# Kernel tuning notes

Hardware: AMD Instinct MI355X
Metric: run time of the kernel (lower is better)

The kernel has to match this reference:

```python
import jax, jax.numpy as jnp
import numpy as np

H = 128          # hid_feats
IN0, IN1 = 128, 64
OUT = 64         # out_feats
L = 3            # num_layers
N = 50000        # nodes per graph


def _rbf(x, W, b):
    # sklearn RBFSampler: z = sqrt(2/D) * cos(x @ W + b)
    return jnp.sqrt(2.0 / H) * jnp.cos(x @ W + b)


def _sage_branch(feat, src, dst, Wself, Wneigh, bias, n_nodes):
    # deg of each dst node (constant across layers)
    deg = jax.ops.segment_sum(jnp.ones_like(dst, dtype=feat.dtype), dst, n_nodes)
    denom = jnp.maximum(deg, 1.0)[:, None]
    for i in range(Wself.shape[0]):
        s = jax.ops.segment_sum(feat[src], dst, n_nodes)   # gather + scatter-add
        neigh = jnp.where(deg[:, None] > 0, s / denom, 0.0)
        feat = feat @ Wself[i] + neigh @ Wneigh[i] + bias[i]
    return feat


def setup_inputs() -> dict:
    key = jax.random.key(0)
    ks = jax.random.split(key, 20)
    gamma = 0.1
    inp = {}
    inp['feat0'] = jax.random.normal(ks[0], (N, IN0), jnp.float32)
    inp['feat1'] = jax.random.normal(ks[1], (N, IN1), jnp.float32)
    E = 800000
    inp['src0'] = jax.random.randint(ks[2], (E,), 0, N, jnp.int32)
    inp['dst0'] = jax.random.randint(ks[3], (E,), 0, N, jnp.int32)
    inp['src1'] = jax.random.randint(ks[4], (E,), 0, N, jnp.int32)
    inp['dst1'] = jax.random.randint(ks[5], (E,), 0, N, jnp.int32)
    # RBF random Fourier feature params (W ~ sqrt(2*gamma)*N(0,1), b ~ U[0,2pi))
    inp['rbf_W0'] = jnp.sqrt(2 * gamma) * jax.random.normal(ks[6], (IN0, H), jnp.float32)
    inp['rbf_b0'] = jax.random.uniform(ks[7], (H,), jnp.float32, 0.0, 2 * np.pi)
    inp['rbf_W1'] = jnp.sqrt(2 * gamma) * jax.random.normal(ks[8], (IN1, H), jnp.float32)
    inp['rbf_b1'] = jax.random.uniform(ks[9], (H,), jnp.float32, 0.0, 2 * np.pi)
    sc = 1.0 / np.sqrt(H)
    # branch 1 (g1) and branch 2 (g0) SAGEConv params, stacked over layers
    inp['Wself1'] = sc * jax.random.normal(ks[10], (L, H, H), jnp.float32)
    inp['Wneigh1'] = sc * jax.random.normal(ks[11], (L, H, H), jnp.float32)
    inp['b1'] = jnp.zeros((L, H), jnp.float32)
    inp['Wself2'] = sc * jax.random.normal(ks[12], (L, H, H), jnp.float32)
    inp['Wneigh2'] = sc * jax.random.normal(ks[13], (L, H, H), jnp.float32)
    inp['b2'] = jnp.zeros((L, H), jnp.float32)
    inp['fc1_W'] = sc * jax.random.normal(ks[14], (2 * H, H), jnp.float32)
    inp['fc1_b'] = jnp.zeros((H,), jnp.float32)
    inp['out_W'] = sc * jax.random.normal(ks[15], (H, OUT), jnp.float32)
    inp['out_b'] = jnp.zeros((OUT,), jnp.float32)
    inp['ro_W'] = (1.0 / np.sqrt(OUT)) * jax.random.normal(ks[16], (OUT, 1), jnp.float32)
    inp['ro_b'] = jnp.zeros((1,), jnp.float32)
    return inp


def reference(feat0, feat1, src0, dst0, src1, dst1,
              rbf_W0, rbf_b0, rbf_W1, rbf_b1,
              Wself1, Wneigh1, b1, Wself2, Wneigh2, b2,
              fc1_W, fc1_b, out_W, out_b, ro_W, ro_b):
    # branch 1: g1 path-complex features
    h1 = _rbf(feat1, rbf_W1, rbf_b1)
    y1 = _sage_branch(h1, src1, dst1, Wself1, Wneigh1, b1, feat1.shape[0])
    # branch 2: g0 node features
    h0 = _rbf(feat0, rbf_W0, rbf_b0)
    y2 = _sage_branch(h0, src0, dst0, Wself2, Wneigh2, b2, feat0.shape[0])
    # adaptive_avg_pool1d to 1 == mean over nodes
    y = jnp.concatenate([y2.mean(axis=0), y1.mean(axis=0)], axis=0)  # [2H]
    h = jax.nn.relu(y @ fc1_W + fc1_b)          # dropout is identity in eval
    h = jax.nn.leaky_relu(h @ out_W + out_b, negative_slope=0.01)
    return h @ ro_W + ro_b                      # [1]
```

## Files before the change

### kernel.cpp

```cpp
#include <hip/hip_runtime.h>
#include <math.h>

#define HF   128
#define CAPW 64
#define HB   64

__global__ __launch_bounds__(256) void histgemm_kernel(const float* __restrict__ A,
                                                       const float* __restrict__ W,
                                                       const float* __restrict__ bias,
                                                       float* __restrict__ hout,
                                                       float* __restrict__ partial,
                                                       const int* __restrict__ s0, const int* __restrict__ d0,
                                                       const int* __restrict__ s1, const int* __restrict__ d1,
                                                       unsigned int* __restrict__ cntbuf,
                                                       int N, int E, int histBlocks){
  __shared__ __align__(16) unsigned int sm32[12544];

  const int t = threadIdx.x;
  const int HW = (N + 3) >> 2;

  if ((int)blockIdx.x < histBlocks){
    const int bid = blockIdx.x;
    const int b  = bid & 63;
    const int br = (bid >> 6) & 1;
    const int z  = bid >> 7;
    const int* keys = z ? (br ? d1 : d0) : (br ? s1 : s0);
    for (int w = t; w < HW; w += 256) sm32[w] = 0u;
    __syncthreads();
    const int C  = (E + HB - 1) / HB;
    const int lo = b * C;
    int hi = lo + C; if (hi > E) hi = E;
    for (int i = lo + t; i < hi; i += 256){
      int k = keys[i];
      atomicAdd(&sm32[k >> 2], 1u << ((k & 3) << 3));
    }
    __syncthreads();
    unsigned int* out = cntbuf + ((size_t)(z * 2 + br) * HB + b) * HW;
    for (int w = t; w < HW; w += 256) out[w] = sm32[w];
    return;
  }

  float (*As)[68]   = (float(*)[68])sm32;
  float (*Bs)[132]  = (float(*)[132])((float*)sm32 + 1088);
  float (*red)[128] = (float(*)[128])sm32;
  const int tx = t & 15;
  const int ty = t >> 4;
  const int rb = (int)blockIdx.x - histBlocks;
  const int rowbase = rb << 6;

  float acc[4][8];
  #pragma unroll
  for (int i = 0; i < 4; ++i)
    #pragma unroll
    for (int j = 0; j < 8; ++j) acc[i][j] = 0.f;

  const int ar = t >> 2;
  const int ac = (t & 3) << 2;
  const int arow = rowbase + ar;
  const int bk0 = t >> 5;
  const int bc0 = (t & 31) << 2;

  for (int k0 = 0; k0 < 128; k0 += 16){
    __syncthreads();
    float4 av = make_float4(0.f, 0.f, 0.f, 0.f);
    if (arow < N) av = *(const float4*)&A[(size_t)arow * 128 + (k0 + ac)];
    As[ac + 0][ar] = av.x; As[ac + 1][ar] = av.y;
    As[ac + 2][ar] = av.z; As[ac + 3][ar] = av.w;
    float4 b0 = *(const float4*)&W[(size_t)(k0 + bk0) * HF + bc0];
    float4 b1 = *(const float4*)&W[(size_t)(k0 + bk0 + 8) * HF + bc0];
    *(float4*)&Bs[bk0][bc0]     = b0;
    *(float4*)&Bs[bk0 + 8][bc0] = b1;
    __syncthreads();
    #pragma unroll
    for (int kk = 0; kk < 16; ++kk){
      const float4 a  = *(const float4*)&As[kk][ty << 2];
      const float4 p0 = *(const float4*)&Bs[kk][tx << 2];
      const float4 p1 = *(const float4*)&Bs[kk][64 + (tx << 2)];
      const float aa[4] = {a.x, a.y, a.z, a.w};
      const float bb[8] = {p0.x, p0.y, p0.z, p0.w, p1.x, p1.y, p1.z, p1.w};
      #pragma unroll
      for (int i = 0; i < 4; ++i)
        #pragma unroll
        for (int j = 0; j < 8; ++j)
          acc[i][j] = fmaf(aa[i], bb[j], acc[i][j]);
    }
  }

  const float4 bia0 = *(const float4*)&bias[tx << 2];
  const float4 bia1 = *(const float4*)&bias[64 + (tx << 2)];
  const float bb0[8] = {bia0.x, bia0.y, bia0.z, bia0.w, bia1.x, bia1.y, bia1.z, bia1.w};
  float o[4][8];
  float cw[8];
  #pragma unroll
  for (int j = 0; j < 8; ++j) cw[j] = 0.f;
  #pragma unroll
  for (int i = 0; i < 4; ++i){
    int row = rowbase + (ty << 2) + i;
    bool valid = row < N;
    #pragma unroll
    for (int j = 0; j < 8; ++j){
      o[i][j] = 0.125f * cosf(acc[i][j] + bb0[j]);
      if (valid) cw[j] += o[i][j];
    }
    if (valid){
      *(float4*)&hout[(size_t)row * HF + (tx << 2)]      = make_float4(o[i][0], o[i][1], o[i][2], o[i][3]);
      *(float4*)&hout[(size_t)row * HF + 64 + (tx << 2)] = make_float4(o[i][4], o[i][5], o[i][6], o[i][7]);
    }
  }

  __syncthreads();
  #pragma unroll
  for (int j = 0; j < 4; ++j){
    red[ty][(tx << 2) + j]      = cw[j];
    red[ty][64 + (tx << 2) + j] = cw[4 + j];
  }
  __syncthreads();
  for (int off = 8; off; off >>= 1){
    if (ty < off){
      #pragma unroll
      for (int j = 0; j < 4; ++j){
        red[ty][(tx << 2) + j]      += red[ty + off][(tx << 2) + j];
        red[ty][64 + (tx << 2) + j] += red[ty + off][64 + (tx << 2) + j];
      }
    }
    __syncthreads();
  }
  if (ty == 0){
    #pragma unroll
    for (int j = 0; j < 4; ++j){
      partial[(size_t)rb * 512 + (tx << 2) + j]      = red[0][(tx << 2) + j];
      partial[(size_t)rb * 512 + 64 + (tx << 2) + j] = red[0][64 + (tx << 2) + j];
    }
  }
}

__global__ __launch_bounds__(256) void scan_kernel(unsigned int* __restrict__ cntbuf,
                                                   int* __restrict__ deg,
                                                   int* __restrict__ fill, int N){
  int k = blockIdx.x * 256 + threadIdx.x;
  if (k >= 2 * N) return;
  const int br = k >= N;
  const int kk = k - br * N;
  const int HW = (N + 3) >> 2;
  unsigned char* cb = (unsigned char*)cntbuf;
  size_t dbase = ((size_t)(2 + br) * HB) * HW * 4 + kk;
  int ds = 0;
  for (int b = 0; b < HB; ++b) ds += cb[dbase + (size_t)b * HW * 4];
  deg[k] = ds;
  size_t sbase = ((size_t)(0 + br) * HB) * HW * 4 + kk;
  int run = 0;
  for (int b = 0; b < HB; ++b){
    size_t a = sbase + (size_t)b * HW * 4;
    int c = cb[a];
    cb[a] = (unsigned char)run;
    run += c;
  }
  fill[k] = run;
}

__global__ __launch_bounds__(256) void scatter_kernel(const int* __restrict__ s0, const int* __restrict__ d0,
                                                      const int* __restrict__ s1, const int* __restrict__ d1,
                                                      const unsigned int* __restrict__ cntbuf,
                                                      unsigned short* __restrict__ slots,
                                                      int N, int E){
  __shared__ unsigned int sm32[12544];
  const int t  = threadIdx.x;
  const int b  = blockIdx.x & 63;
  const int br = blockIdx.x >> 6;
  const int HW = (N + 3) >> 2;
  const unsigned int* offw = cntbuf + ((size_t)br * HB + b) * HW;
  for (int w = t; w < HW; w += 256) sm32[w] = offw[w];
  __syncthreads();
  const int* srcA = br ? s1 : s0;
  const int* dstA = br ? d1 : d0;
  const int C  = (E + HB - 1) / HB;
  const int lo = b * C;
  int hi = lo + C; if (hi > E) hi = E;
  const size_t obase = (size_t)br * N;
  for (int i = lo + t; i < hi; i += 256){
    int s = srcA[i];
    int d = dstA[i];
    unsigned int old = atomicAdd(&sm32[s >> 2], 1u << ((s & 3) << 3));
    int j = (old >> ((s & 3) << 3)) & 0xff;
    if (j < CAPW) slots[(obase + s) * CAPW + j] = (unsigned short)d;
  }
}

__global__ __launch_bounds__(256) void pull1_kernel(const unsigned short* __restrict__ slots,
                                                    const int* __restrict__ fill,
                                                    const int* __restrict__ deg,
                                                    float* __restrict__ w1,
                                                    float* __restrict__ qa,
                                                    double* __restrict__ S, int N){
  int i = blockIdx.x * 256 + threadIdx.x;
  int t = threadIdx.x;
  float a = 0.f;
  int dgi = 0;
  int br = 0;
  bool valid = i < 2 * N;
  if (valid){
    br = i >= N;
    int o = br * N;
    int c = fill[i]; if (c > CAPW) c = CAPW;
    const unsigned short* sl = slots + (size_t)i * CAPW;
    int j = 0;
    for (; j + 3 < c; j += 4){
      int dA = sl[j], dB = sl[j+1], dC = sl[j+2], dD = sl[j+3];
      a += 1.f/(float)deg[o+dA] + 1.f/(float)deg[o+dB]
         + 1.f/(float)deg[o+dC] + 1.f/(float)deg[o+dD];
    }
    for (; j < c; ++j) a += 1.f/(float)deg[o + sl[j]];
    dgi = deg[i];
    w1[i] = a;
    qa[i] = dgi > 0 ? a * (1.f/(float)dgi) : 0.f;
  }
  __shared__ double rd[4][256];
  bool pos = valid && dgi > 0;
  rd[0][t] = (pos && !br) ? 1.0 : 0.0;
  rd[1][t] = (pos && !br) ? (double)a : 0.0;
  rd[2][t] = (pos &&  br) ? 1.0 : 0.0;
  rd[3][t] = (pos &&  br) ? (double)a : 0.0;
  __syncthreads();
  for (int off = 128; off; off >>= 1){
    if (t < off){
      rd[0][t] += rd[0][t+off]; rd[1][t] += rd[1][t+off];
      rd[2][t] += rd[2][t+off]; rd[3][t] += rd[3][t+off];
    }
    __syncthreads();
  }
  if (t < 4) atomicAdd(&S[t], rd[t][0]);
}

template<bool WQ>
__global__ __launch_bounds__(256) void pull_kernel(const unsigned short* __restrict__ slots,
                                                   const int* __restrict__ fill,
                                                   const int* __restrict__ deg,
                                                   const float* __restrict__ qin,
                                                   float* __restrict__ wout,
                                                   float* __restrict__ qout, int N){
  int i = blockIdx.x * 256 + threadIdx.x;
  if (i >= 2 * N) return;
  int br = i >= N;
  int o = br * N;
  int c = fill[i]; if (c > CAPW) c = CAPW;
  const unsigned short* sl = slots + (size_t)i * CAPW;
  float a = 0.f;
  int j = 0;
  for (; j + 3 < c; j += 4){
    int dA = sl[j], dB = sl[j+1], dC = sl[j+2], dD = sl[j+3];
    a += qin[o+dA] + qin[o+dB] + qin[o+dC] + qin[o+dD];
  }
  for (; j < c; ++j) a += qin[o + sl[j]];
  wout[i] = a;
  if (WQ){
    int dgi = deg[i];
    qout[i] = dgi > 0 ? a * (1.f/(float)dgi) : 0.f;
  }
}

__global__ __launch_bounds__(256) void tail_kernel(const float* __restrict__ A1,
                                                   const float* __restrict__ W1,
                                                   const float* __restrict__ bias1,
                                                   const float* __restrict__ h0,
                                                   const float* __restrict__ w1,
                                                   const float* __restrict__ w2,
                                                   const float* __restrict__ w3,
                                                   float* __restrict__ partial0,
                                                   float* __restrict__ partial1,
                                                   int N, int gg){
  __shared__ __align__(16) float smem[3200];
  float (*As)[68]   = (float(*)[68])smem;
  float (*Bs)[132]  = (float(*)[132])(smem + 1088);
  float (*red)[128] = (float(*)[128])smem;
  const int t  = threadIdx.x;
  const int tx = t & 15;
  const int ty = t >> 4;

  if ((int)blockIdx.x >= gg){
    const int wb = blockIdx.x - gg;
    const int rowbase = wb << 6;
    float o[4][8];
    float wr[3][4];
    #pragma unroll
    for (int i = 0; i < 4; ++i){
      int row = rowbase + (ty << 2) + i;
      bool valid = row < N;
      float4 x0 = make_float4(0,0,0,0), x1 = make_float4(0,0,0,0);
      if (valid){
        x0 = *(const float4*)&h0[(size_t)row * HF + (tx << 2)];
        x1 = *(const float4*)&h0[(size_t)row * HF + 64 + (tx << 2)];
      }
      o[i][0]=x0.x; o[i][1]=x0.y; o[i][2]=x0.z; o[i][3]=x0.w;
      o[i][4]=x1.x; o[i][5]=x1.y; o[i][6]=x1.z; o[i][7]=x1.w;
      wr[0][i] = valid ? w1[row] : 0.f;
      wr[1][i] = valid ? w2[row] : 0.f;
      wr[2][i] = valid ? w3[row] : 0.f;
    }
    #pragma unroll
    for (int k = 0; k < 3; ++k){
      float cw[8];
      #pragma unroll
      for (int j = 0; j < 8; ++j)
        cw[j] = wr[k][0]*o[0][j] + wr[k][1]*o[1][j] + wr[k][2]*o[2][j] + wr[k][3]*o[3][j];
      __syncthreads();
      #pragma unroll
      for (int j = 0; j < 4; ++j){
        red[ty][(tx << 2) + j]      = cw[j];
        red[ty][64 + (tx << 2) + j] = cw[4 + j];
      }
      __syncthreads();
      for (int off = 8; off; off >>= 1){
        if (ty < off){
          #pragma unroll
          for (int j = 0; j < 4; ++j){
            red[ty][(tx << 2) + j]      += red[ty + off][(tx << 2) + j];
            red[ty][64 + (tx << 2) + j] += red[ty + off][64 + (tx << 2) + j];
          }
        }
        __syncthreads();
      }
      if (ty == 0){
        #pragma unroll
        for (int j = 0; j < 4; ++j){
          partial0[(size_t)wb * 512 + (k + 1) * 128 + (tx << 2) + j]      = red[0][(tx << 2) + j];
          partial0[(size_t)wb * 512 + (k + 1) * 128 + 64 + (tx << 2) + j] = red[0][64 + (tx << 2) + j];
        }
      }
      __syncthreads();
    }
    return;
  }

  const int rowbase = (int)blockIdx.x << 6;
  float acc[4][8];
  #pragma unroll
  for (int i = 0; i < 4; ++i)
    #pragma unroll
    for (int j = 0; j < 8; ++j) acc[i][j] = 0.f;

  const int ar = t >> 2;
  const int ac = (t & 3) << 2;
  const int arow = rowbase + ar;
  const int bk0 = t >> 5;
  const int bc0 = (t & 31) << 2;

  for (int k0 = 0; k0 < 64; k0 += 16){
    __syncthreads();
    float4 av = make_float4(0.f, 0.f, 0.f, 0.f);
    if (arow < N) av = *(const float4*)&A1[(size_t)arow * 64 + (k0 + ac)];
    As[ac + 0][ar] = av.x; As[ac + 1][ar] = av.y;
    As[ac + 2][ar] = av.z; As[ac + 3][ar] = av.w;
    float4 b0 = *(const float4*)&W1[(size_t)(k0 + bk0) * HF + bc0];
    float4 b1 = *(const float4*)&W1[(size_t)(k0 + bk0 + 8) * HF + bc0];
    *(float4*)&Bs[bk0][bc0]     = b0;
    *(float4*)&Bs[bk0 + 8][bc0] = b1;
    __syncthreads();
    #pragma unroll
    for (int kk = 0; kk < 16; ++kk){
      const float4 a  = *(const float4*)&As[kk][ty << 2];
      const float4 p0 = *(const float4*)&Bs[kk][tx << 2];
      const float4 p1 = *(const float4*)&Bs[kk][64 + (tx << 2)];
      const float aa[4] = {a.x, a.y, a.z, a.w};
      const float bb[8] = {p0.x, p0.y, p0.z, p0.w, p1.x, p1.y, p1.z, p1.w};
      #pragma unroll
      for (int i = 0; i < 4; ++i)
        #pragma unroll
        for (int j = 0; j < 8; ++j)
          acc[i][j] = fmaf(aa[i], bb[j], acc[i][j]);
    }
  }

  const float4 bia0 = *(const float4*)&bias1[tx << 2];
  const float4 bia1 = *(const float4*)&bias1[64 + (tx << 2)];
  const float bb0[8] = {bia0.x, bia0.y, bia0.z, bia0.w, bia1.x, bia1.y, bia1.z, bia1.w};
  float o[4][8];
  float wr[4][4];
  #pragma unroll
  for (int i = 0; i < 4; ++i){
    int row = rowbase + (ty << 2) + i;
    bool valid = row < N;
    #pragma unroll
    for (int j = 0; j < 8; ++j)
      o[i][j] = 0.125f * cosf(acc[i][j] + bb0[j]);
    wr[0][i] = valid ? 1.f : 0.f;
    wr[1][i] = valid ? w1[N + row] : 0.f;
    wr[2][i] = valid ? w2[N + row] : 0.f;
    wr[3][i] = valid ? w3[N + row] : 0.f;
  }
  __syncthreads();
  #pragma unroll
  for (int k = 0; k < 4; ++k){
    float cw[8];
    #pragma unroll
    for (int j = 0; j < 8; ++j)
      cw[j] = wr[k][0]*o[0][j] + wr[k][1]*o[1][j] + wr[k][2]*o[2][j] + wr[k][3]*o[3][j];
    #pragma unroll
    for (int j = 0; j < 4; ++j){
      red[ty][(tx << 2) + j]      = cw[j];
      red[ty][64 + (tx << 2) + j] = cw[4 + j];
    }
    __syncthreads();
    for (int off = 8; off; off >>= 1){
      if (ty < off){
        #pragma unroll
        for (int j = 0; j < 4; ++j){
          red[ty][(tx << 2) + j]      += red[ty + off][(tx << 2) + j];
          red[ty][64 + (tx << 2) + j] += red[ty + off][64 + (tx << 2) + j];
        }
      }
      __syncthreads();
    }
    if (ty == 0){
      #pragma unroll
      for (int j = 0; j < 4; ++j){
        partial1[(size_t)blockIdx.x * 512 + k * 128 + (tx << 2) + j]      = red[0][(tx << 2) + j];
        partial1[(size_t)blockIdx.x * 512 + k * 128 + 64 + (tx << 2) + j] = red[0][64 + (tx << 2) + j];
      }
    }
    __syncthreads();
  }
}

__global__ __launch_bounds__(512) void greduce_kernel(const float* __restrict__ partial,
                                                      double* __restrict__ G, int nb, int stride){
  int br = blockIdx.y;
  const float* p = partial + (size_t)br * stride;
  double* Gb = G + 512 * br;
  int t = threadIdx.x;
  double s = 0.0;
  for (int b = blockIdx.x; b < nb; b += gridDim.x) s += (double)p[(size_t)b * 512 + t];
  atomicAdd(&Gb[t], s);
}

__global__ __launch_bounds__(512) void head_kernel(const double* __restrict__ G,
                                                   const double* __restrict__ S,
                                                   const float* __restrict__ WsA, const float* __restrict__ WnA, const float* __restrict__ bA,
                                                   const float* __restrict__ WsB, const float* __restrict__ WnB, const float* __restrict__ bB,
                                                   float* __restrict__ ymean, int n){
  const int br = blockIdx.x;
  const double* Gb = G + 512 * br;
  const double* Sb = S + 2 * br;
  const float* Ws   = br ? WsB : WsA;
  const float* Wn   = br ? WnB : WnA;
  const float* bias = br ? bB  : bA;
  float* yout = ymean + 128 * br;

  __shared__ double g[4][128], ng[3][128];
  __shared__ float lws[32][128], lwn[32][128];
  const int t = threadIdx.x;
  const int k = t >> 7, j = t & 127;
  g[k][j] = Gb[t];
  double s[4];
  s[0] = (double)n; s[1] = Sb[0]; s[2] = Sb[1]; s[3] = 0.0;

  for (int i = 0; i < 3; ++i){
    const float* ws = Ws + (size_t)i * 16384;
    const float* wn = Wn + (size_t)i * 16384;
    const float* bi = bias + (size_t)i * 128;
    const int kmax = 2 - i;
    double a = (k <= kmax) ? s[k] * (double)bi[j] : 0.0;
    for (int mc = 0; mc < 128; mc += 32){
      __syncthreads();
      #pragma unroll
      for (int p = 0; p < 2; ++p){
        int idx = (p * 512 + t) << 2;
        int mm = idx >> 7, cc = idx & 127;
        *(float4*)&lws[mm][cc] = *(const float4*)&ws[(size_t)(mc + mm) * 128 + cc];
        *(float4*)&lwn[mm][cc] = *(const float4*)&wn[(size_t)(mc + mm) * 128 + cc];
      }
      __syncthreads();
      if (k <= kmax){
        #pragma unroll
        for (int m = 0; m < 32; ++m){
          a += g[k][mc + m]     * (double)lws[m][j];
          a += g[k + 1][mc + m] * (double)lwn[m][j];
        }
      }
    }
    __syncthreads();
    if (k <= kmax) ng[k][j] = a;
    __syncthreads();
    if (k <= kmax) g[k][j] = ng[k][j];
  }
  __syncthreads();
  if (t < 128) yout[t] = (float)(g[0][t] / (double)n);
}

__global__ void final_kernel(const float* __restrict__ ymean,
                             const float* __restrict__ fc1W, const float* __restrict__ fc1b,
                             const float* __restrict__ outW, const float* __restrict__ outb,
                             const float* __restrict__ roW, const float* __restrict__ rob,
                             float* __restrict__ out){
  __shared__ float y[256], h1[128], h2[64];
  int t = threadIdx.x;
  y[t] = ymean[t];
  __syncthreads();
  if (t < 128){
    float a = fc1b[t];
    for (int k = 0; k < 256; ++k) a = fmaf(y[k], fc1W[k * 128 + t], a);
    h1[t] = a > 0.f ? a : 0.f;
  }
  __syncthreads();
  if (t < 64){
    float a = outb[t];
    for (int k = 0; k < 128; ++k) a = fmaf(h1[k], outW[k * 64 + t], a);
    h2[t] = a > 0.f ? a : 0.01f * a;
  }
  __syncthreads();
  if (t == 0){
    float a = rob[0];
    for (int k = 0; k < 64; ++k) a = fmaf(h2[k], roW[k], a);
    out[0] = a;
  }
}

extern "C" void kernel_launch(void* const* d_in, const int* in_sizes, int n_in,
                              void* d_out, int out_size, void* d_ws, size_t ws_size,
                              hipStream_t stream){
  const float* feat0  = (const float*)d_in[0];
  const float* feat1  = (const float*)d_in[1];
  const int*   src0   = (const int*)d_in[2];
  const int*   dst0   = (const int*)d_in[3];
  const int*   src1   = (const int*)d_in[4];
  const int*   dst1   = (const int*)d_in[5];
  const float* rbfW0  = (const float*)d_in[6];
  const float* rbfb0  = (const float*)d_in[7];
  const float* rbfW1  = (const float*)d_in[8];
  const float* rbfb1  = (const float*)d_in[9];
  const float* Wself1 = (const float*)d_in[10];
  const float* Wneigh1= (const float*)d_in[11];
  const float* b1     = (const float*)d_in[12];
  const float* Wself2 = (const float*)d_in[13];
  const float* Wneigh2= (const float*)d_in[14];
  const float* b2     = (const float*)d_in[15];
  const float* fc1W   = (const float*)d_in[16];
  const float* fc1b   = (const float*)d_in[17];
  const float* outW   = (const float*)d_in[18];
  const float* outb   = (const float*)d_in[19];
  const float* roW    = (const float*)d_in[20];
  const float* rob    = (const float*)d_in[21];

  const int N = in_sizes[0] / 128;
  const int E = in_sizes[2];
  const int HW = (N + 3) >> 2;

  char* w = (char*)d_ws;
  size_t off = 0;
  auto alloc = [&](size_t bytes) -> char* {
    char* p = w + off; off += (bytes + 255) & ~(size_t)255; return p;
  };
  int*    deg    = (int*)   alloc((size_t)2 * N * 4);
  int*    fill   = (int*)   alloc((size_t)2 * N * 4);
  float*  w1     = (float*) alloc((size_t)2 * N * 4);
  float*  w2     = (float*) alloc((size_t)2 * N * 4);
  float*  w3     = (float*) alloc((size_t)2 * N * 4);
  float*  qa     = (float*) alloc((size_t)2 * N * 4);
  float*  qb     = (float*) alloc((size_t)2 * N * 4);
  double* S      = (double*)alloc(4 * sizeof(double));
  double* G      = (double*)alloc(1024 * sizeof(double));
  float*  ymean  = (float*) alloc(256 * sizeof(float));
  const int gg   = (N + 63) >> 6;
  float*  partial= (float*) alloc((size_t)2 * gg * 512 * 4);
  float*  h0buf  = (float*) alloc((size_t)N * HF * 4);
  unsigned short* slots = (unsigned short*)alloc((size_t)2 * N * CAPW * 2);
  unsigned int* cntbuf  = (unsigned int*)alloc((size_t)4 * HB * HW * 4);

  const size_t slen = (size_t)((char*)ymean - (char*)S);

  const int nGrid2 = (2 * N + 255) >> 8;

  hipMemsetAsync(S, 0, slen, stream);
  histgemm_kernel<<<256 + gg, 256, 0, stream>>>(feat0, rbfW0, rbfb0, h0buf, partial,
                                                src0, dst0, src1, dst1, cntbuf, N, E, 256);
  scan_kernel<<<nGrid2, 256, 0, stream>>>(cntbuf, deg, fill, N);
  scatter_kernel<<<128, 256, 0, stream>>>(src0, dst0, src1, dst1, cntbuf, slots, N, E);
  pull1_kernel<<<nGrid2, 256, 0, stream>>>(slots, fill, deg, w1, qa, S, N);
  pull_kernel<true ><<<nGrid2, 256, 0, stream>>>(slots, fill, deg, qa, w2, qb, N);
  pull_kernel<false><<<nGrid2, 256, 0, stream>>>(slots, fill, deg, qb, w3, qb, N);
  tail_kernel<<<2 * gg, 256, 0, stream>>>(feat1, rbfW1, rbfb1, h0buf, w1, w2, w3,
                                          partial, partial + (size_t)gg * 512, N, gg);
  greduce_kernel<<<dim3(16, 2), 512, 0, stream>>>(partial, G, gg, gg * 512);
  head_kernel<<<2, 512, 0, stream>>>(G, S, Wself2, Wneigh2, b2, Wself1, Wneigh1, b1, ymean, N);
  final_kernel<<<1, 256, 0, stream>>>(ymean, fc1W, fc1b, outW, outb, roW, rob, (float*)d_out);
}
```

Baseline: 216.1 us.

## Halve histogram LDS via two-pass key ranges, unroll pulls, fold greduce into head

The histogram blocks now count keys in two halves of the node range with half the shared memory, rereading the keys once per half. The smaller static LDS allocation is meant to let more GEMM and histogram blocks co-reside. The pull kernels unroll their gather loops by eight instead of four for more memory-level parallelism. The separate greduce kernel and its memset region are removed, and head_kernel now sums the per-block partials itself serially over about 782 blocks with only two workgroups, which may be slower than the parallel reduction it replaces.

```diff
diff --git a/kernel.cpp b/kernel.cpp
--- a/kernel.cpp
+++ b/kernel.cpp
@@ -14,10 +14,12 @@
                                                        const int* __restrict__ s1, const int* __restrict__ d1,
                                                        unsigned int* __restrict__ cntbuf,
                                                        int N, int E, int histBlocks){
-  __shared__ __align__(16) unsigned int sm32[12544];
+  __shared__ __align__(16) unsigned int sm32[6272];
 
   const int t = threadIdx.x;
   const int HW = (N + 3) >> 2;
+  const int HN = ((N + 7) >> 3) << 2;
+  const int W0 = HN >> 2;
 
   if ((int)blockIdx.x < histBlocks){
     const int bid = blockIdx.x;
@@ -25,18 +27,28 @@
     const int br = (bid >> 6) & 1;
     const int z  = bid >> 7;
     const int* keys = z ? (br ? d1 : d0) : (br ? s1 : s0);
-    for (int w = t; w < HW; w += 256) sm32[w] = 0u;
-    __syncthreads();
     const int C  = (E + HB - 1) / HB;
     const int lo = b * C;
     int hi = lo + C; if (hi > E) hi = E;
-    for (int i = lo + t; i < hi; i += 256){
-      int k = keys[i];
-      atomicAdd(&sm32[k >> 2], 1u << ((k & 3) << 3));
-    }
-    __syncthreads();
     unsigned int* out = cntbuf + ((size_t)(z * 2 + br) * HB + b) * HW;
-    for (int w = t; w < HW; w += 256) out[w] = sm32[w];
+    #pragma unroll
+    for (int h = 0; h < 2; ++h){
+      const int klo = h ? HN : 0;
+      const int khi = h ? N : HN;
+      const int nw = (khi - klo + 3) >> 2;
+      for (int w = t; w < nw; w += 256) sm32[w] = 0u;
+      __syncthreads();
+      for (int i = lo + t; i < hi; i += 256){
+        int k = keys[i];
+        if (k >= klo && k < khi){
+          int kl = k - klo;
+          atomicAdd(&sm32[kl >> 2], 1u << ((kl & 3) << 3));
+        }
+      }
+      __syncthreads();
+      for (int w = t; w < nw; w += 256) out[h * W0 + w] = sm32[w];
+      __syncthreads();
+    }
     return;
   }
 
@@ -204,10 +216,13 @@
     int c = fill[i]; if (c > CAPW) c = CAPW;
     const unsigned short* sl = slots + (size_t)i * CAPW;
     int j = 0;
-    for (; j + 3 < c; j += 4){
+    for (; j + 7 < c; j += 8){
       int dA = sl[j], dB = sl[j+1], dC = sl[j+2], dD = sl[j+3];
+      int dE = sl[j+4], dF = sl[j+5], dG = sl[j+6], dH = sl[j+7];
       a += 1.f/(float)deg[o+dA] + 1.f/(float)deg[o+dB]
-         + 1.f/(float)deg[o+dC] + 1.f/(float)deg[o+dD];
+         + 1.f/(float)deg[o+dC] + 1.f/(float)deg[o+dD]
+         + 1.f/(float)deg[o+dE] + 1.f/(float)deg[o+dF]
+         + 1.f/(float)deg[o+dG] + 1.f/(float)deg[o+dH];
     }
     for (; j < c; ++j) a += 1.f/(float)deg[o + sl[j]];
     dgi = deg[i];
@@ -246,9 +261,11 @@
   const unsigned short* sl = slots + (size_t)i * CAPW;
   float a = 0.f;
   int j = 0;
-  for (; j + 3 < c; j += 4){
+  for (; j + 7 < c; j += 8){
     int dA = sl[j], dB = sl[j+1], dC = sl[j+2], dD = sl[j+3];
-    a += qin[o+dA] + qin[o+dB] + qin[o+dC] + qin[o+dD];
+    int dE = sl[j+4], dF = sl[j+5], dG = sl[j+6], dH = sl[j+7];
+    a += qin[o+dA] + qin[o+dB] + qin[o+dC] + qin[o+dD]
+       + qin[o+dE] + qin[o+dF] + qin[o+dG] + qin[o+dH];
   }
   for (; j < c; ++j) a += qin[o + sl[j]];
   wout[i] = a;
@@ -421,24 +438,13 @@
   }
 }
 
-__global__ __launch_bounds__(512) void greduce_kernel(const float* __restrict__ partial,
-                                                      double* __restrict__ G, int nb, int stride){
-  int br = blockIdx.y;
-  const float* p = partial + (size_t)br * stride;
-  double* Gb = G + 512 * br;
-  int t = threadIdx.x;
-  double s = 0.0;
-  for (int b = blockIdx.x; b < nb; b += gridDim.x) s += (double)p[(size_t)b * 512 + t];
-  atomicAdd(&Gb[t], s);
-}
-
-__global__ __launch_bounds__(512) void head_kernel(const double* __restrict__ G,
+__global__ __launch_bounds__(512) void head_kernel(const float* __restrict__ partial,
                                                    const double* __restrict__ S,
                                                    const float* __restrict__ WsA, const float* __restrict__ WnA, const float* __restrict__ bA,
                                                    const float* __restrict__ WsB, const float* __restrict__ WnB, const float* __restrict__ bB,
-                                                   float* __restrict__ ymean, int n){
+                                                   float* __restrict__ ymean, int gg, int n){
   const int br = blockIdx.x;
-  const double* Gb = G + 512 * br;
+  const float* p = partial + (size_t)br * gg * 512;
   const double* Sb = S + 2 * br;
   const float* Ws   = br ? WsB : WsA;
   const float* Wn   = br ? WnB : WnA;
@@ -449,7 +455,15 @@
   __shared__ float lws[32][128], lwn[32][128];
   const int t = threadIdx.x;
   const int k = t >> 7, j = t & 127;
-  g[k][j] = Gb[t];
+
+  double acc = 0.0;
+  int b = 0;
+  for (; b + 3 < gg; b += 4){
+    acc += (double)p[(size_t)b * 512 + t] + (double)p[(size_t)(b+1) * 512 + t]
+         + (double)p[(size_t)(b+2) * 512 + t] + (double)p[(size_t)(b+3) * 512 + t];
+  }
+  for (; b < gg; ++b) acc += (double)p[(size_t)b * 512 + t];
+  g[k][j] = acc;
   double s[4];
   s[0] = (double)n; s[1] = Sb[0]; s[2] = Sb[1]; s[3] = 0.0;
 
@@ -462,8 +476,8 @@
     for (int mc = 0; mc < 128; mc += 32){
       __syncthreads();
       #pragma unroll
-      for (int p = 0; p < 2; ++p){
-        int idx = (p * 512 + t) << 2;
+      for (int pp = 0; pp < 2; ++pp){
+        int idx = (pp * 512 + t) << 2;
         int mm = idx >> 7, cc = idx & 127;
         *(float4*)&lws[mm][cc] = *(const float4*)&ws[(size_t)(mc + mm) * 128 + cc];
         *(float4*)&lwn[mm][cc] = *(const float4*)&wn[(size_t)(mc + mm) * 128 + cc];
@@ -557,7 +571,6 @@
   float*  qa     = (float*) alloc((size_t)2 * N * 4);
   float*  qb     = (float*) alloc((size_t)2 * N * 4);
   double* S      = (double*)alloc(4 * sizeof(double));
-  double* G      = (double*)alloc(1024 * sizeof(double));
   float*  ymean  = (float*) alloc(256 * sizeof(float));
   const int gg   = (N + 63) >> 6;
   float*  partial= (float*) alloc((size_t)2 * gg * 512 * 4);
@@ -565,11 +578,9 @@
   unsigned short* slots = (unsigned short*)alloc((size_t)2 * N * CAPW * 2);
   unsigned int* cntbuf  = (unsigned int*)alloc((size_t)4 * HB * HW * 4);
 
-  const size_t slen = (size_t)((char*)ymean - (char*)S);
-
   const int nGrid2 = (2 * N + 255) >> 8;
 
-  hipMemsetAsync(S, 0, slen, stream);
+  hipMemsetAsync(S, 0, 4 * sizeof(double), stream);
   histgemm_kernel<<<256 + gg, 256, 0, stream>>>(feat0, rbfW0, rbfb0, h0buf, partial,
                                                 src0, dst0, src1, dst1, cntbuf, N, E, 256);
   scan_kernel<<<nGrid2, 256, 0, stream>>>(cntbuf, deg, fill, N);
@@ -579,7 +590,7 @@
   pull_kernel<false><<<nGrid2, 256, 0, stream>>>(slots, fill, deg, qb, w3, qb, N);
   tail_kernel<<<2 * gg, 256, 0, stream>>>(feat1, rbfW1, rbfb1, h0buf, w1, w2, w3,
                                           partial, partial + (size_t)gg * 512, N, gg);
-  greduce_kernel<<<dim3(16, 2), 512, 0, stream>>>(partial, G, gg, gg * 512);
-  head_kernel<<<2, 512, 0, stream>>>(G, S, Wself2, Wneigh2, b2, Wself1, Wneigh1, b1, ymean, N);
+  head_kernel<<<2, 512, 0, stream>>>(partial, S, Wself2, Wneigh2, b2, Wself1, Wneigh1, b1,
+                                     ymean, gg, N);
   final_kernel<<<1, 256, 0, stream>>>(ymean, fc1W, fc1b, outW, outb, roW, rob, (float*)d_out);
 }
```

New measurement: 255.2 us. +18.1%, slower.
